# Kernel tuning notes

Hardware: AMD Instinct MI355X
Metric: run time of the kernel (lower is better)

Reference implementation:

```python
import jax, jax.numpy as jnp
import numpy as np

B, N, DIM, H = 32, 3136, 768, 12
C = DIM // H  # head_dim = 64


def setup_inputs() -> dict:
    key = jax.random.key(0)
    k1, k2, k3, k4 = jax.random.split(key, 4)
    x = jax.random.normal(k1, (B, N, DIM), dtype=jnp.float32)
    # Linear weights stored as (in, out); qkv has no bias (qkv_bias=False)
    w_qkv = jax.random.normal(k2, (DIM, 3 * DIM), dtype=jnp.float32) * (1.0 / np.sqrt(DIM))
    w_proj = jax.random.normal(k3, (DIM, DIM), dtype=jnp.float32) * (1.0 / np.sqrt(DIM))
    b_proj = jax.random.normal(k4, (DIM,), dtype=jnp.float32) * 0.01
    return {"x": x, "w_qkv": w_qkv, "w_proj": w_proj, "b_proj": b_proj}


def reference(x, w_qkv, w_proj, b_proj):
    # qkv projection: [B,N,3*DIM] -> [3,B,H,N,C]
    qkv = (x @ w_qkv).reshape(B, N, 3, H, C).transpose(2, 0, 3, 1, 4)
    q, k, v = qkv[0], qkv[1], qkv[2]
    # Efficient (linear) attention: softmax q over channel dim, k over token dim
    q = jax.nn.softmax(q, axis=-1)                      # [B,H,N,C], softmax over C
    kt = jax.nn.softmax(k.transpose(0, 1, 3, 2), axis=-1)  # [B,H,C,N], softmax over N
    context = jnp.einsum('bhcn,bhnd->bhcd', kt, v)      # [B,H,C,C]
    out = jnp.einsum('bhnc,bhcd->bhnd', q, context)     # [B,H,N,C]
    out = out.transpose(0, 2, 1, 3).reshape(B, N, DIM)  # [B,N,DIM]
    return out @ w_proj + b_proj
```

## Files before the change

### kernel.cpp

```cpp
#include <hip/hip_runtime.h>
#include <hip/hip_bf16.h>

typedef __attribute__((ext_vector_type(8))) short bf16x8;
typedef __attribute__((ext_vector_type(4))) float f32x4;

constexpr int BATCH = 32, SEQ = 3136, DIM = 768, NH = 12, HD = 64;
constexpr int M_TOT = BATCH * SEQ;
constexpr int QKVC  = 3 * DIM;
constexpr int GK    = 768;

__device__ __forceinline__ float bf2f(unsigned short u) {
  union { unsigned int i; float f; } x; x.i = ((unsigned int)u) << 16; return x.f;
}
__device__ __forceinline__ unsigned short f2bf(float f) {
  union { float f; unsigned int i; } x; x.f = f;
  unsigned int r = x.i + 0x7FFFu + ((x.i >> 16) & 1u);
  return (unsigned short)(r >> 16);
}
__device__ __forceinline__ unsigned int pack2(float lo, float hi) {
  return (unsigned int)f2bf(lo) | ((unsigned int)f2bf(hi) << 16);
}
__device__ __forceinline__ void gload_lds16(const unsigned short* g, unsigned short* l) {
  __builtin_amdgcn_global_load_lds(
      (const __attribute__((address_space(1))) void*)g,
      (__attribute__((address_space(3))) void*)l, 16, 0, 0);
}

#define BARX()  asm volatile("s_barrier" ::: "memory")
#define LGKM0() asm volatile("s_waitcnt lgkmcnt(0)" ::: "memory")
#define VM8()   asm volatile("s_waitcnt vmcnt(8)" ::: "memory")
#define VM6()   asm volatile("s_waitcnt vmcnt(6)" ::: "memory")
#define SB0()   __builtin_amdgcn_sched_barrier(0)

__global__ void prep_kernel(const float* __restrict__ x, unsigned short* __restrict__ x_bf,
                            const float* __restrict__ w_qkv, unsigned short* __restrict__ wt_qkv,
                            const float* __restrict__ w_proj, unsigned short* __restrict__ wt_proj) {
  __shared__ float tile[32][33];
  int bid = blockIdx.x, t = threadIdx.x;
  if (bid < 2048) {
    long n = (long)M_TOT * DIM;
    long i = ((long)bid * 256 + t) * 8;
    long stride = (long)2048 * 256 * 8;
    for (; i < n; i += stride) {
      float4 a = *(const float4*)(x + i);
      float4 b = *(const float4*)(x + i + 4);
      uint4 o;
      o.x = pack2(a.x, a.y); o.y = pack2(a.z, a.w);
      o.z = pack2(b.x, b.y); o.w = pack2(b.z, b.w);
      *(uint4*)(x_bf + i) = o;
    }
  } else {
    const float* w; unsigned short* wt; int N, bx, by;
    if (bid < 2048 + 1728) {
      int r = bid - 2048; w = w_qkv; wt = wt_qkv; N = QKVC; bx = r % 72; by = r / 72;
    } else {
      int r = bid - 3776; w = w_proj; wt = wt_proj; N = DIM; bx = r % 24; by = r / 24;
    }
    int n0 = bx * 32, k0 = by * 32;
    int tx = t & 31, ty = t >> 5;
    #pragma unroll
    for (int i = 0; i < 32; i += 8)
      tile[ty + i][tx] = w[(size_t)(k0 + ty + i) * N + n0 + tx];
    __syncthreads();
    #pragma unroll
    for (int i = 0; i < 32; i += 8)
      wt[(size_t)(n0 + ty + i) * GK + k0 + tx] = f2bf(tile[tx][ty + i]);
  }
}

__device__ __forceinline__ void stage_half(const unsigned short* __restrict__ G, long row0, int col0,
                                           unsigned short* ldsHalf, int t) {
  int r = t >> 2;
  int gslot = (t & 3) ^ ((t >> 3) & 3);
  char* dst = (char*)ldsHalf + ((t >> 6) << 10);
  gload_lds16(G + (row0 + r) * (long)GK + col0 + gslot * 8, (unsigned short*)dst);
  gload_lds16(G + (row0 + 128 + r) * (long)GK + col0 + gslot * 8, (unsigned short*)(dst + 8192));
}
__device__ __forceinline__ bf16x8 frag(const unsigned short* half, int r, int ko) {
  return *(const bf16x8*)((const char*)half + r * 64 + ((((ko >> 3) ^ ((r >> 1) & 3))) << 4));
}

#define MM16G(Q,A0,A1,A2,A3,B0,B1,B2,B3) do { \
  acc[(Q)+0][0]=__builtin_amdgcn_mfma_f32_16x16x32_bf16(B0,A0,acc[(Q)+0][0],0,0,0); \
  acc[(Q)+0][1]=__builtin_amdgcn_mfma_f32_16x16x32_bf16(B1,A0,acc[(Q)+0][1],0,0,0); \
  acc[(Q)+0][2]=__builtin_amdgcn_mfma_f32_16x16x32_bf16(B2,A0,acc[(Q)+0][2],0,0,0); \
  acc[(Q)+0][3]=__builtin_amdgcn_mfma_f32_16x16x32_bf16(B3,A0,acc[(Q)+0][3],0,0,0); \
  acc[(Q)+1][0]=__builtin_amdgcn_mfma_f32_16x16x32_bf16(B0,A1,acc[(Q)+1][0],0,0,0); \
  acc[(Q)+1][1]=__builtin_amdgcn_mfma_f32_16x16x32_bf16(B1,A1,acc[(Q)+1][1],0,0,0); \
  acc[(Q)+1][2]=__builtin_amdgcn_mfma_f32_16x16x32_bf16(B2,A1,acc[(Q)+1][2],0,0,0); \
  acc[(Q)+1][3]=__builtin_amdgcn_mfma_f32_16x16x32_bf16(B3,A1,acc[(Q)+1][3],0,0,0); \
  acc[(Q)+2][0]=__builtin_amdgcn_mfma_f32_16x16x32_bf16(B0,A2,acc[(Q)+2][0],0,0,0); \
  acc[(Q)+2][1]=__builtin_amdgcn_mfma_f32_16x16x32_bf16(B1,A2,acc[(Q)+2][1],0,0,0); \
  acc[(Q)+2][2]=__builtin_amdgcn_mfma_f32_16x16x32_bf16(B2,A2,acc[(Q)+2][2],0,0,0); \
  acc[(Q)+2][3]=__builtin_amdgcn_mfma_f32_16x16x32_bf16(B3,A2,acc[(Q)+2][3],0,0,0); \
  acc[(Q)+3][0]=__builtin_amdgcn_mfma_f32_16x16x32_bf16(B0,A3,acc[(Q)+3][0],0,0,0); \
  acc[(Q)+3][1]=__builtin_amdgcn_mfma_f32_16x16x32_bf16(B1,A3,acc[(Q)+3][1],0,0,0); \
  acc[(Q)+3][2]=__builtin_amdgcn_mfma_f32_16x16x32_bf16(B2,A3,acc[(Q)+3][2],0,0,0); \
  acc[(Q)+3][3]=__builtin_amdgcn_mfma_f32_16x16x32_bf16(B3,A3,acc[(Q)+3][3],0,0,0); \
} while (0)

#define KTILE_W(BUF, MA2, NB2, C2, MA3, NB3, C3) { \
  const unsigned short* Ah0 = &lds[BUF][0][0][0]; \
  const unsigned short* Bh1 = &lds[BUF][1][1][0]; \
  const unsigned short* Ah1 = &lds[BUF][0][1][0]; \
  const unsigned short* Ah0n = &lds[(BUF) ^ 1][0][0][0]; \
  const unsigned short* Bh0n = &lds[(BUF) ^ 1][1][0][0]; \
   \
  LGKM0(); SB0(); \
  __builtin_amdgcn_s_setprio(1); MM16G(0, a0, a1, a2, a3, b0, b1, b2, b3); \
  __builtin_amdgcn_s_setprio(0); SB0(); \
  a4 = frag(Ah0, ra + 64, ko); a5 = frag(Ah0, ra + 80, ko); \
  a6 = frag(Ah0, ra + 96, ko); a7 = frag(Ah0, ra + 112, ko); \
  stage_half(A, MA2, C2, &lds[(BUF) ^ 1][0][1][0], t); \
  VM6(); BARX(); \
   \
  LGKM0(); SB0(); \
  __builtin_amdgcn_s_setprio(1); MM16G(4, a4, a5, a6, a7, b0, b1, b2, b3); \
  __builtin_amdgcn_s_setprio(0); SB0(); \
  a0 = frag(Ah1, ra,      ko); a1 = frag(Ah1, ra + 16, ko); \
  a2 = frag(Ah1, ra + 32, ko); a3 = frag(Ah1, ra + 48, ko); \
  b4 = frag(Bh1, rb,      ko); b5 = frag(Bh1, rb + 16, ko); \
  b6 = frag(Bh1, rb + 32, ko); b7 = frag(Bh1, rb + 48, ko); \
  stage_half(Bt, NB2, C2, &lds[(BUF) ^ 1][1][1][0], t); \
  BARX(); \
   \
  LGKM0(); SB0(); \
  __builtin_amdgcn_s_setprio(1); MM16G(0, a0, a1, a2, a3, b4, b5, b6, b7); \
  __builtin_amdgcn_s_setprio(0); SB0(); \
  a4 = frag(Ah1, ra + 64, ko); a5 = frag(Ah1, ra + 80, ko); \
  a6 = frag(Ah1, ra + 96, ko); a7 = frag(Ah1, ra + 112, ko); \
  stage_half(A, MA3, C3, &lds[BUF][0][0][0], t); \
  VM6(); BARX(); \
   \
  LGKM0(); SB0(); \
  __builtin_amdgcn_s_setprio(1); MM16G(4, a4, a5, a6, a7, b4, b5, b6, b7); \
  __builtin_amdgcn_s_setprio(0); SB0(); \
  a0 = frag(Ah0n, ra,      ko); a1 = frag(Ah0n, ra + 16, ko); \
  a2 = frag(Ah0n, ra + 32, ko); a3 = frag(Ah0n, ra + 48, ko); \
  b0 = frag(Bh0n, rb,      ko); b1 = frag(Bh0n, rb + 16, ko); \
  b2 = frag(Bh0n, rb + 32, ko); b3 = frag(Bh0n, rb + 48, ko); \
  stage_half(Bt, NB3, C3, &lds[BUF][1][0][0], t); \
  BARX(); \
}

template<int OUTMODE, int NT>
__global__ __launch_bounds__(512, 2) void gemm256p(const unsigned short* __restrict__ A,
                                                   const unsigned short* __restrict__ Bt,
                                                   void* __restrict__ Cp,
                                                   const float* __restrict__ bias,
                                                   int Nld, int TPX) {
  __shared__ unsigned short lds[2][2][2][8192];
  int t = threadIdx.x, lane = t & 63, wid = t >> 6;
  int wm = wid >> 2, wn = wid & 3;
  int bid = (int)blockIdx.x;
  int xcd = bid & 7, slot = bid >> 3;
  int tau = xcd * TPX + slot;
  int tend = (xcd + 1) * TPX;
  int fl = lane & 15, ko = (lane >> 4) * 8;
  int ra = wm * 128 + fl, rb = wn * 64 + fl;
  f32x4 acc[8][4];
  bf16x8 a0, a1, a2, a3, a4, a5, a6, a7, b0, b1, b2, b3, b4, b5, b6, b7;
  {
    long m0 = (long)(tau / NT) * 256, n0 = (long)(tau % NT) * 256;
    stage_half(A,  m0, 0,  &lds[0][0][0][0], t);
    stage_half(Bt, n0, 0,  &lds[0][1][0][0], t);
    stage_half(A,  m0, 32, &lds[0][0][1][0], t);
    stage_half(Bt, n0, 32, &lds[0][1][1][0], t);
    stage_half(A,  m0, 64, &lds[1][0][0][0], t);
    stage_half(Bt, n0, 64, &lds[1][1][0][0], t);
    VM8(); BARX();
    a0 = frag(&lds[0][0][0][0], ra,      ko); a1 = frag(&lds[0][0][0][0], ra + 16, ko);
    a2 = frag(&lds[0][0][0][0], ra + 32, ko); a3 = frag(&lds[0][0][0][0], ra + 48, ko);
    b0 = frag(&lds[0][1][0][0], rb,      ko); b1 = frag(&lds[0][1][0][0], rb + 16, ko);
    b2 = frag(&lds[0][1][0][0], rb + 32, ko); b3 = frag(&lds[0][1][0][0], rb + 48, ko);
  }
  #pragma unroll 1
  for (; tau < tend; tau += 32) {
    long m0 = (long)(tau / NT) * 256, n0 = (long)(tau % NT) * 256;
    int tn = (tau + 32 < tend) ? tau + 32 : tau;
    long m0n = (long)(tn / NT) * 256, n0n = (long)(tn % NT) * 256;
    #pragma unroll
    for (int i = 0; i < 8; ++i)
      #pragma unroll
      for (int j2 = 0; j2 < 4; ++j2) acc[i][j2] = (f32x4){0.f, 0.f, 0.f, 0.f};
    #pragma unroll 1
    for (int j = 0; j < 10; j += 2) {
      KTILE_W(0, m0, n0, j * 64 + 96,  m0, n0, j * 64 + 128);
      KTILE_W(1, m0, n0, j * 64 + 160, m0, n0, j * 64 + 192);
    }
    KTILE_W(0, m0,  n0,  736, m0n, n0n, 0);
    KTILE_W(1, m0n, n0n, 32,  m0n, n0n, 64);
    int q4 = (lane >> 4) * 4;
    #pragma unroll
    for (int mf = 0; mf < 8; ++mf) {
      long row = m0 + wm * 128 + mf * 16 + fl;
      #pragma unroll
      for (int nf = 0; nf < 4; ++nf) {
        int col = (int)n0 + wn * 64 + nf * 16 + q4;
        if (OUTMODE == 0) {
          unsigned short* C = (unsigned short*)Cp;
          bool doexp = (n0 < 2 * DIM);
          float v0 = acc[mf][nf][0], v1 = acc[mf][nf][1], v2 = acc[mf][nf][2], v3 = acc[mf][nf][3];
          if (doexp) { v0 = __expf(v0); v1 = __expf(v1); v2 = __expf(v2); v3 = __expf(v3); }
          uint2 o; o.x = pack2(v0, v1); o.y = pack2(v2, v3);
          *(uint2*)(C + (size_t)row * Nld + col) = o;
        } else {
          float* C = (float*)Cp;
          float4 bb = *(const float4*)(bias + col);
          float4 o = { acc[mf][nf][0] + bb.x, acc[mf][nf][1] + bb.y,
                       acc[mf][nf][2] + bb.z, acc[mf][nf][3] + bb.w };
          *(float4*)(C + (size_t)row * Nld + col) = o;
        }
      }
    }
  }
}

__global__ void ctx_part(const unsigned short* __restrict__ qkv, float* __restrict__ part,
                         float* __restrict__ dpart) {
  int blk = blockIdx.x;
  int bh = blk / 7, ch = blk - bh * 7;
  int b = bh / NH, h = bh % NH;
  __shared__ unsigned short Et[64 * 40];
  __shared__ unsigned short Vt[64 * 40];
  __shared__ float denom[64];
  int t = threadIdx.x, lane = t & 63, w = t >> 6;
  if (t < 64) denom[t] = 0.0f;
  int nl = t >> 3, e0 = (t & 7) * 8;
  int ko = (lane >> 4) * 8, fl = lane & 15;
  size_t base = (size_t)b * SEQ * QKVC + (size_t)h * HD;
  float dp[8] = {};
  f32x4 acc[4] = {};
  int c0b = ch * 448;
  for (int c0 = c0b; c0 < c0b + 448; c0 += 32) {
    __syncthreads();
    size_t rb = base + (size_t)(c0 + nl) * QKVC;
    uint4 kvec = *(const uint4*)(qkv + rb + DIM + e0);
    uint4 vvec = *(const uint4*)(qkv + rb + 2 * DIM + e0);
    const unsigned short* kp = (const unsigned short*)&kvec;
    const unsigned short* vp = (const unsigned short*)&vvec;
    #pragma unroll
    for (int j = 0; j < 8; ++j) {
      dp[j] += bf2f(kp[j]);
      Et[(e0 + j) * 40 + nl] = kp[j];
      Vt[(e0 + j) * 40 + nl] = vp[j];
    }
    __syncthreads();
    bf16x8 af = *(const bf16x8*)(Et + (w * 16 + fl) * 40 + ko);
    #pragma unroll
    for (int nf = 0; nf < 4; ++nf) {
      bf16x8 bv = *(const bf16x8*)(Vt + (nf * 16 + fl) * 40 + ko);
      acc[nf] = __builtin_amdgcn_mfma_f32_16x16x32_bf16(af, bv, acc[nf], 0, 0, 0);
    }
  }
  #pragma unroll
  for (int j = 0; j < 8; ++j) atomicAdd(&denom[e0 + j], dp[j]);
  __syncthreads();
  int r0 = (lane >> 4) * 4;
  float* pp = part + (size_t)blk * 4096;
  #pragma unroll
  for (int nf = 0; nf < 4; ++nf)
    #pragma unroll
    for (int r = 0; r < 4; ++r) {
      int c = w * 16 + r0 + r;
      int d = nf * 16 + fl;
      pp[d * 64 + c] = acc[nf][r];
    }
  if (t < 64) dpart[blk * 64 + t] = denom[t];
}

__global__ void ctx_reduce(const float* __restrict__ part, const float* __restrict__ dpart,
                           unsigned short* __restrict__ ctxT) {
  int bh = blockIdx.x, t = threadIdx.x;
  const float* pp = part + (size_t)bh * 7 * 4096;
  const float* dd = dpart + (size_t)bh * 7 * 64;
  #pragma unroll
  for (int i = 0; i < 16; ++i) {
    int idx = i * 256 + t;
    float s = 0.f, ds = 0.f;
    #pragma unroll
    for (int c = 0; c < 7; ++c) {
      s += pp[c * 4096 + idx];
      ds += dd[c * 64 + (idx & 63)];
    }
    ctxT[(size_t)bh * 4096 + idx] = f2bf(s / ds);
  }
}

__global__ void pv_kernel(const unsigned short* __restrict__ qkv, const unsigned short* __restrict__ ctxT,
                          unsigned short* __restrict__ aout) {
  int bid = blockIdx.x;
  int bh = bid / 49, chunk = bid - bh * 49;
  int b = bh / NH, h = bh % NH;
  int n0 = chunk * 64;
  __shared__ unsigned short P[64 * 80];
  __shared__ unsigned short CT[64 * 80];
  __shared__ float srow[64];
  int t = threadIdx.x, lane = t & 63, w = t >> 6;
  int ko = (lane >> 4) * 8, fl = lane & 15;
  if (t < 64) srow[t] = 0.0f;
  {
    int d = t >> 2, cq = (t & 3) * 16;
    const uint4* src = (const uint4*)(ctxT + (size_t)bh * 4096 + d * 64 + cq);
    *(uint4*)(CT + d * 80 + cq) = src[0];
    *(uint4*)(CT + d * 80 + cq + 8) = src[1];
  }
  __syncthreads();
  {
    int nl = t >> 2, cq = (t & 3) * 16;
    size_t rb = (size_t)(b * SEQ + n0 + nl) * QKVC + h * HD + cq;
    uint4 q0 = *(const uint4*)(qkv + rb);
    uint4 q1 = *(const uint4*)(qkv + rb + 8);
    *(uint4*)(P + nl * 80 + cq) = q0;
    *(uint4*)(P + nl * 80 + cq + 8) = q1;
    const unsigned short* qp0 = (const unsigned short*)&q0;
    const unsigned short* qp1 = (const unsigned short*)&q1;
    float s = 0.0f;
    #pragma unroll
    for (int j = 0; j < 8; ++j) s += bf2f(qp0[j]) + bf2f(qp1[j]);
    atomicAdd(&srow[nl], s);
  }
  __syncthreads();
  f32x4 acc[4] = {};
  #pragma unroll
  for (int kk = 0; kk < 2; ++kk) {
    bf16x8 af = *(const bf16x8*)(P + (w * 16 + fl) * 80 + kk * 32 + ko);
    #pragma unroll
    for (int nf = 0; nf < 4; ++nf) {
      bf16x8 bv = *(const bf16x8*)(CT + (nf * 16 + fl) * 80 + kk * 32 + ko);
      acc[nf] = __builtin_amdgcn_mfma_f32_16x16x32_bf16(af, bv, acc[nf], 0, 0, 0);
    }
  }
  int r0 = (lane >> 4) * 4;
  #pragma unroll
  for (int nf = 0; nf < 4; ++nf)
    #pragma unroll
    for (int r = 0; r < 4; ++r) {
      int nlr = w * 16 + r0 + r;
      int d = nf * 16 + fl;
      float v = acc[nf][r] / srow[nlr];
      aout[(size_t)(b * SEQ + n0 + nlr) * DIM + h * HD + d] = f2bf(v);
    }
}

extern "C" void kernel_launch(void* const* d_in, const int* in_sizes, int n_in,
                              void* d_out, int out_size, void* d_ws, size_t ws_size,
                              hipStream_t stream) {
  const float* x      = (const float*)d_in[0];
  const float* w_qkv  = (const float*)d_in[1];
  const float* w_proj = (const float*)d_in[2];
  const float* b_proj = (const float*)d_in[3];
  char* ws = (char*)d_ws;
  unsigned short* x_bf    = (unsigned short*)(ws);
  unsigned short* wt_qkv  = (unsigned short*)(ws + 154140672);
  unsigned short* wt_proj = (unsigned short*)(ws + 157679616);
  unsigned short* qkv     = (unsigned short*)(ws + 158859264);
  unsigned short* ctxT    = (unsigned short*)(ws + 154140672);
  float* part  = (float*)(ws);
  float* dpart = (float*)(ws + 44040192);
  unsigned short* aout = (unsigned short*)(ws);

  prep_kernel<<<4352, 256, 0, stream>>>(x, x_bf, w_qkv, wt_qkv, w_proj, wt_proj);
  gemm256p<0, 9><<<256, 512, 0, stream>>>(x_bf, wt_qkv, qkv, nullptr, QKVC, 441);
  ctx_part<<<BATCH * NH * 7, 256, 0, stream>>>(qkv, part, dpart);
  ctx_reduce<<<BATCH * NH, 256, 0, stream>>>(part, dpart, ctxT);
  pv_kernel<<<BATCH * NH * (SEQ / 64), 256, 0, stream>>>(qkv, ctxT, aout);
  gemm256p<1, 3><<<256, 512, 0, stream>>>(aout, wt_proj, (float*)d_out, b_proj, DIM, 147);
}
```

Baseline: 858.2 us.

## Switch GEMM inner kernel from 16x16x32 to 32x32x16 MFMA tiles

Replaces the 16x16x32 bf16 MFMA micro-kernel with 32x32x16 MFMA instructions, cutting the number of MFMA issues and LDS fragment reads per k-step (fewer B fragments, 16-wide accumulators). Fragment addressing is reworked for the 32-row layout. The epilogue now writes one scalar element per lane per register instead of vectorized 4-wide stores, which may make output stores less coalesced and more numerous.

```diff
diff --git a/kernel.cpp b/kernel.cpp
--- a/kernel.cpp
+++ b/kernel.cpp
@@ -2,12 +2,14 @@
 #include <hip/hip_bf16.h>
 
 typedef __attribute__((ext_vector_type(8))) short bf16x8;
-typedef __attribute__((ext_vector_type(4))) float f32x4;
+typedef __attribute__((ext_vector_type(16))) float f32x16;
 
 constexpr int BATCH = 32, SEQ = 3136, DIM = 768, NH = 12, HD = 64;
 constexpr int M_TOT = BATCH * SEQ;
 constexpr int QKVC  = 3 * DIM;
 constexpr int GK    = 768;
+
+typedef __attribute__((ext_vector_type(4))) float f32x4;
 
 __device__ __forceinline__ float bf2f(unsigned short u) {
   union { unsigned int i; float f; } x; x.i = ((unsigned int)u) << 16; return x.f;
@@ -76,69 +78,62 @@
   gload_lds16(G + (row0 + r) * (long)GK + col0 + gslot * 8, (unsigned short*)dst);
   gload_lds16(G + (row0 + 128 + r) * (long)GK + col0 + gslot * 8, (unsigned short*)(dst + 8192));
 }
-__device__ __forceinline__ bf16x8 frag(const unsigned short* half, int r, int ko) {
-  return *(const bf16x8*)((const char*)half + r * 64 + ((((ko >> 3) ^ ((r >> 1) & 3))) << 4));
-}
-
-#define MM16G(Q,A0,A1,A2,A3,B0,B1,B2,B3) do { \
-  acc[(Q)+0][0]=__builtin_amdgcn_mfma_f32_16x16x32_bf16(B0,A0,acc[(Q)+0][0],0,0,0); \
-  acc[(Q)+0][1]=__builtin_amdgcn_mfma_f32_16x16x32_bf16(B1,A0,acc[(Q)+0][1],0,0,0); \
-  acc[(Q)+0][2]=__builtin_amdgcn_mfma_f32_16x16x32_bf16(B2,A0,acc[(Q)+0][2],0,0,0); \
-  acc[(Q)+0][3]=__builtin_amdgcn_mfma_f32_16x16x32_bf16(B3,A0,acc[(Q)+0][3],0,0,0); \
-  acc[(Q)+1][0]=__builtin_amdgcn_mfma_f32_16x16x32_bf16(B0,A1,acc[(Q)+1][0],0,0,0); \
-  acc[(Q)+1][1]=__builtin_amdgcn_mfma_f32_16x16x32_bf16(B1,A1,acc[(Q)+1][1],0,0,0); \
-  acc[(Q)+1][2]=__builtin_amdgcn_mfma_f32_16x16x32_bf16(B2,A1,acc[(Q)+1][2],0,0,0); \
-  acc[(Q)+1][3]=__builtin_amdgcn_mfma_f32_16x16x32_bf16(B3,A1,acc[(Q)+1][3],0,0,0); \
-  acc[(Q)+2][0]=__builtin_amdgcn_mfma_f32_16x16x32_bf16(B0,A2,acc[(Q)+2][0],0,0,0); \
-  acc[(Q)+2][1]=__builtin_amdgcn_mfma_f32_16x16x32_bf16(B1,A2,acc[(Q)+2][1],0,0,0); \
-  acc[(Q)+2][2]=__builtin_amdgcn_mfma_f32_16x16x32_bf16(B2,A2,acc[(Q)+2][2],0,0,0); \
-  acc[(Q)+2][3]=__builtin_amdgcn_mfma_f32_16x16x32_bf16(B3,A2,acc[(Q)+2][3],0,0,0); \
-  acc[(Q)+3][0]=__builtin_amdgcn_mfma_f32_16x16x32_bf16(B0,A3,acc[(Q)+3][0],0,0,0); \
-  acc[(Q)+3][1]=__builtin_amdgcn_mfma_f32_16x16x32_bf16(B1,A3,acc[(Q)+3][1],0,0,0); \
-  acc[(Q)+3][2]=__builtin_amdgcn_mfma_f32_16x16x32_bf16(B2,A3,acc[(Q)+3][2],0,0,0); \
-  acc[(Q)+3][3]=__builtin_amdgcn_mfma_f32_16x16x32_bf16(B3,A3,acc[(Q)+3][3],0,0,0); \
+__device__ __forceinline__ bf16x8 frag32(const unsigned short* half, int r, int ck) {
+  return *(const bf16x8*)((const char*)half + r * 64 + ((ck ^ ((r >> 1) & 3)) << 4));
+}
+
+#define MM8(A0,A1,A2,A3,B0,B1) do { \
+  acc[0]=__builtin_amdgcn_mfma_f32_32x32x16_bf16(A0,B0,acc[0],0,0,0); \
+  acc[1]=__builtin_amdgcn_mfma_f32_32x32x16_bf16(A0,B1,acc[1],0,0,0); \
+  acc[2]=__builtin_amdgcn_mfma_f32_32x32x16_bf16(A1,B0,acc[2],0,0,0); \
+  acc[3]=__builtin_amdgcn_mfma_f32_32x32x16_bf16(A1,B1,acc[3],0,0,0); \
+  acc[4]=__builtin_amdgcn_mfma_f32_32x32x16_bf16(A2,B0,acc[4],0,0,0); \
+  acc[5]=__builtin_amdgcn_mfma_f32_32x32x16_bf16(A2,B1,acc[5],0,0,0); \
+  acc[6]=__builtin_amdgcn_mfma_f32_32x32x16_bf16(A3,B0,acc[6],0,0,0); \
+  acc[7]=__builtin_amdgcn_mfma_f32_32x32x16_bf16(A3,B1,acc[7],0,0,0); \
 } while (0)
 
-#define KTILE_W(BUF, MA2, NB2, C2, MA3, NB3, C3) { \
+#define KTILE32(BUF, MA2, NB2, C2, MA3, NB3, C3) { \
   const unsigned short* Ah0 = &lds[BUF][0][0][0]; \
+  const unsigned short* Bh0 = &lds[BUF][1][0][0]; \
+  const unsigned short* Ah1 = &lds[BUF][0][1][0]; \
   const unsigned short* Bh1 = &lds[BUF][1][1][0]; \
-  const unsigned short* Ah1 = &lds[BUF][0][1][0]; \
   const unsigned short* Ah0n = &lds[(BUF) ^ 1][0][0][0]; \
   const unsigned short* Bh0n = &lds[(BUF) ^ 1][1][0][0]; \
    \
   LGKM0(); SB0(); \
-  __builtin_amdgcn_s_setprio(1); MM16G(0, a0, a1, a2, a3, b0, b1, b2, b3); \
+  __builtin_amdgcn_s_setprio(1); MM8(a0, a1, a2, a3, b0, b1); \
   __builtin_amdgcn_s_setprio(0); SB0(); \
-  a4 = frag(Ah0, ra + 64, ko); a5 = frag(Ah0, ra + 80, ko); \
-  a6 = frag(Ah0, ra + 96, ko); a7 = frag(Ah0, ra + 112, ko); \
+  a4 = frag32(Ah0, ra,      ck1); a5 = frag32(Ah0, ra + 32, ck1); \
+  a6 = frag32(Ah0, ra + 64, ck1); a7 = frag32(Ah0, ra + 96, ck1); \
+  b2 = frag32(Bh0, rbr,     ck1); b3 = frag32(Bh0, rbr + 32, ck1); \
   stage_half(A, MA2, C2, &lds[(BUF) ^ 1][0][1][0], t); \
   VM6(); BARX(); \
    \
   LGKM0(); SB0(); \
-  __builtin_amdgcn_s_setprio(1); MM16G(4, a4, a5, a6, a7, b0, b1, b2, b3); \
+  __builtin_amdgcn_s_setprio(1); MM8(a4, a5, a6, a7, b2, b3); \
   __builtin_amdgcn_s_setprio(0); SB0(); \
-  a0 = frag(Ah1, ra,      ko); a1 = frag(Ah1, ra + 16, ko); \
-  a2 = frag(Ah1, ra + 32, ko); a3 = frag(Ah1, ra + 48, ko); \
-  b4 = frag(Bh1, rb,      ko); b5 = frag(Bh1, rb + 16, ko); \
-  b6 = frag(Bh1, rb + 32, ko); b7 = frag(Bh1, rb + 48, ko); \
+  a0 = frag32(Ah1, ra,      ck0); a1 = frag32(Ah1, ra + 32, ck0); \
+  a2 = frag32(Ah1, ra + 64, ck0); a3 = frag32(Ah1, ra + 96, ck0); \
+  b0 = frag32(Bh1, rbr,     ck0); b1 = frag32(Bh1, rbr + 32, ck0); \
   stage_half(Bt, NB2, C2, &lds[(BUF) ^ 1][1][1][0], t); \
   BARX(); \
    \
   LGKM0(); SB0(); \
-  __builtin_amdgcn_s_setprio(1); MM16G(0, a0, a1, a2, a3, b4, b5, b6, b7); \
+  __builtin_amdgcn_s_setprio(1); MM8(a0, a1, a2, a3, b0, b1); \
   __builtin_amdgcn_s_setprio(0); SB0(); \
-  a4 = frag(Ah1, ra + 64, ko); a5 = frag(Ah1, ra + 80, ko); \
-  a6 = frag(Ah1, ra + 96, ko); a7 = frag(Ah1, ra + 112, ko); \
+  a4 = frag32(Ah1, ra,      ck1); a5 = frag32(Ah1, ra + 32, ck1); \
+  a6 = frag32(Ah1, ra + 64, ck1); a7 = frag32(Ah1, ra + 96, ck1); \
+  b2 = frag32(Bh1, rbr,     ck1); b3 = frag32(Bh1, rbr + 32, ck1); \
   stage_half(A, MA3, C3, &lds[BUF][0][0][0], t); \
   VM6(); BARX(); \
    \
   LGKM0(); SB0(); \
-  __builtin_amdgcn_s_setprio(1); MM16G(4, a4, a5, a6, a7, b4, b5, b6, b7); \
+  __builtin_amdgcn_s_setprio(1); MM8(a4, a5, a6, a7, b2, b3); \
   __builtin_amdgcn_s_setprio(0); SB0(); \
-  a0 = frag(Ah0n, ra,      ko); a1 = frag(Ah0n, ra + 16, ko); \
-  a2 = frag(Ah0n, ra + 32, ko); a3 = frag(Ah0n, ra + 48, ko); \
-  b0 = frag(Bh0n, rb,      ko); b1 = frag(Bh0n, rb + 16, ko); \
-  b2 = frag(Bh0n, rb + 32, ko); b3 = frag(Bh0n, rb + 48, ko); \
+  a0 = frag32(Ah0n, ra,      ck0); a1 = frag32(Ah0n, ra + 32, ck0); \
+  a2 = frag32(Ah0n, ra + 64, ck0); a3 = frag32(Ah0n, ra + 96, ck0); \
+  b0 = frag32(Bh0n, rbr,     ck0); b1 = frag32(Bh0n, rbr + 32, ck0); \
   stage_half(Bt, NB3, C3, &lds[BUF][1][0][0], t); \
   BARX(); \
 }
@@ -156,10 +151,11 @@
   int xcd = bid & 7, slot = bid >> 3;
   int tau = xcd * TPX + slot;
   int tend = (xcd + 1) * TPX;
-  int fl = lane & 15, ko = (lane >> 4) * 8;
-  int ra = wm * 128 + fl, rb = wn * 64 + fl;
-  f32x4 acc[8][4];
-  bf16x8 a0, a1, a2, a3, a4, a5, a6, a7, b0, b1, b2, b3, b4, b5, b6, b7;
+  int l31 = lane & 31, lh = lane >> 5;
+  int ck0 = lh, ck1 = 2 + lh;
+  int ra = wm * 128 + l31, rbr = wn * 64 + l31;
+  f32x16 acc[8];
+  bf16x8 a0, a1, a2, a3, a4, a5, a6, a7, b0, b1, b2, b3;
   {
     long m0 = (long)(tau / NT) * 256, n0 = (long)(tau % NT) * 256;
     stage_half(A,  m0, 0,  &lds[0][0][0][0], t);
@@ -169,10 +165,9 @@
     stage_half(A,  m0, 64, &lds[1][0][0][0], t);
     stage_half(Bt, n0, 64, &lds[1][1][0][0], t);
     VM8(); BARX();
-    a0 = frag(&lds[0][0][0][0], ra,      ko); a1 = frag(&lds[0][0][0][0], ra + 16, ko);
-    a2 = frag(&lds[0][0][0][0], ra + 32, ko); a3 = frag(&lds[0][0][0][0], ra + 48, ko);
-    b0 = frag(&lds[0][1][0][0], rb,      ko); b1 = frag(&lds[0][1][0][0], rb + 16, ko);
-    b2 = frag(&lds[0][1][0][0], rb + 32, ko); b3 = frag(&lds[0][1][0][0], rb + 48, ko);
+    a0 = frag32(&lds[0][0][0][0], ra,      ck0); a1 = frag32(&lds[0][0][0][0], ra + 32, ck0);
+    a2 = frag32(&lds[0][0][0][0], ra + 64, ck0); a3 = frag32(&lds[0][0][0][0], ra + 96, ck0);
+    b0 = frag32(&lds[0][1][0][0], rbr,     ck0); b1 = frag32(&lds[0][1][0][0], rbr + 32, ck0);
   }
   #pragma unroll 1
   for (; tau < tend; tau += 32) {
@@ -182,34 +177,38 @@
     #pragma unroll
     for (int i = 0; i < 8; ++i)
       #pragma unroll
-      for (int j2 = 0; j2 < 4; ++j2) acc[i][j2] = (f32x4){0.f, 0.f, 0.f, 0.f};
+      for (int j2 = 0; j2 < 16; ++j2) acc[i][j2] = 0.f;
     #pragma unroll 1
     for (int j = 0; j < 10; j += 2) {
-      KTILE_W(0, m0, n0, j * 64 + 96,  m0, n0, j * 64 + 128);
-      KTILE_W(1, m0, n0, j * 64 + 160, m0, n0, j * 64 + 192);
-    }
-    KTILE_W(0, m0,  n0,  736, m0n, n0n, 0);
-    KTILE_W(1, m0n, n0n, 32,  m0n, n0n, 64);
-    int q4 = (lane >> 4) * 4;
-    #pragma unroll
-    for (int mf = 0; mf < 8; ++mf) {
-      long row = m0 + wm * 128 + mf * 16 + fl;
+      KTILE32(0, m0, n0, j * 64 + 96,  m0, n0, j * 64 + 128);
+      KTILE32(1, m0, n0, j * 64 + 160, m0, n0, j * 64 + 192);
+    }
+    KTILE32(0, m0,  n0,  736, m0n, n0n, 0);
+    KTILE32(1, m0n, n0n, 32,  m0n, n0n, 64);
+    #pragma unroll
+    for (int rb2 = 0; rb2 < 4; ++rb2) {
       #pragma unroll
-      for (int nf = 0; nf < 4; ++nf) {
-        int col = (int)n0 + wn * 64 + nf * 16 + q4;
+      for (int cb = 0; cb < 2; ++cb) {
+        f32x16 v = acc[rb2 * 2 + cb];
+        int col = (int)n0 + wn * 64 + cb * 32 + l31;
+        long rowb = m0 + wm * 128 + rb2 * 32 + lh * 4;
         if (OUTMODE == 0) {
           unsigned short* C = (unsigned short*)Cp;
           bool doexp = (n0 < 2 * DIM);
-          float v0 = acc[mf][nf][0], v1 = acc[mf][nf][1], v2 = acc[mf][nf][2], v3 = acc[mf][nf][3];
-          if (doexp) { v0 = __expf(v0); v1 = __expf(v1); v2 = __expf(v2); v3 = __expf(v3); }
-          uint2 o; o.x = pack2(v0, v1); o.y = pack2(v2, v3);
-          *(uint2*)(C + (size_t)row * Nld + col) = o;
+          #pragma unroll
+          for (int reg = 0; reg < 16; ++reg) {
+            long row = rowb + (reg & 3) + 8 * (reg >> 2);
+            float x = v[reg];
+            C[(size_t)row * Nld + col] = f2bf(doexp ? __expf(x) : x);
+          }
         } else {
           float* C = (float*)Cp;
-          float4 bb = *(const float4*)(bias + col);
-          float4 o = { acc[mf][nf][0] + bb.x, acc[mf][nf][1] + bb.y,
-                       acc[mf][nf][2] + bb.z, acc[mf][nf][3] + bb.w };
-          *(float4*)(C + (size_t)row * Nld + col) = o;
+          float bb = bias[col];
+          #pragma unroll
+          for (int reg = 0; reg < 16; ++reg) {
+            long row = rowb + (reg & 3) + 8 * (reg >> 2);
+            C[(size_t)row * Nld + col] = v[reg] + bb;
+          }
         }
       }
     }
```

Measured after the change: 835.7 us. 1.03x faster.
